# Optimization experiments

Measured on AMD Instinct MI355X. Metric: run time of the kernel, lower is better.

Reference implementation:

```python
import jax, jax.numpy as jnp
import numpy as np

B, H, D, N = 4, 16, 64, 2048

def setup_inputs() -> dict:
    key = jax.random.key(0)
    kq, kk, kv = jax.random.split(key, 3)
    q = jax.random.normal(kq, (B, H, D, N), dtype=jnp.float32)
    k = jax.random.normal(kk, (B, H, D, N), dtype=jnp.float32)
    v = jax.random.normal(kv, (B, H, D, N), dtype=jnp.float32)
    return {"q": q, "k": k, "v": v}

def reference(q, k, v):
    # layout: (b, h, d, n); scale uses head_dim = q.shape[-2]
    scale = q.shape[-2] ** (-0.5)
    sim = jnp.einsum('bhdi,bhdj->bhij', q * scale, k)  # [B,H,N,N]
    attn = jax.nn.softmax(sim, axis=-1)  # stable softmax (internally subtracts max)
    out = jnp.einsum('bhij,bhdj->bhdi', attn, v)  # [B,H,D,N]
    return out
```

## Files before the change

kernel.cpp:

```cpp
#include <hip/hip_runtime.h>


#define DDIM 64
#define NSEQ 2048
#define STR  72
#define BUFB (128 * STR * 2)

typedef _Float16 half8   __attribute__((ext_vector_type(8)));
typedef _Float16 half4v  __attribute__((ext_vector_type(4)));
typedef _Float16 half2v  __attribute__((ext_vector_type(2)));
typedef float    float4v __attribute__((ext_vector_type(4)));

__global__ __launch_bounds__(1024, 4) void attn_fwd(
    const float* __restrict__ qg, const float* __restrict__ kg,
    const float* __restrict__ vg, float* __restrict__ og) {
  __shared__ __align__(16) char smem[4 * BUFB];

  const int t    = threadIdx.x;
  const int lane = t & 63;
  const int w    = t >> 6;
  const int n16  = lane & 15;
  const int quad = lane >> 4;

  const int bid  = blockIdx.x;
  const int head = ((bid & 7) << 3) | (bid >> 5);
  const int tile = (bid >> 3) & 3;
  const int i0   = tile * 512;

  const float* qh = qg + (size_t)head * DDIM * NSEQ;
  const float* kh = kg + (size_t)head * DDIM * NSEQ;
  const float* vh = vg + (size_t)head * DDIM * NSEQ;

  const int  u   = t & 511;
  const bool isK = (t < 512);
  const int  dp  = u & 31;
  const int  iq  = u >> 5;
  const int  vd  = u >> 3;
  const int  sj  = u & 7;
  const int  vg_ = sj >> 2;
  const int  vq  = sj & 3;

  const float* kp  = kh + (2 * dp) * NSEQ + iq * 4;
  const float* vpA = vh + vd * NSEQ + vg_ * 32 + vq * 4;

  float4v ra, rb;
  if (isK) { ra = *(const float4v*)(kp);  rb = *(const float4v*)(kp + NSEQ); }
  else     { ra = *(const float4v*)(vpA); rb = *(const float4v*)(vpA + 16);  }

  {
    _Float16* Qt = (_Float16*)smem;
    const float mul = 0.125f * 1.44269504088896340736f;
    const int dpq = t & 31;
    const int ic  = t >> 5;
#pragma unroll
    for (int h = 0; h < 4; ++h) {
      const float* r0 = qh + (2 * dpq) * NSEQ + i0 + h * 128 + ic * 4;
      float4v a = *(const float4v*)(r0);
      float4v b = *(const float4v*)(r0 + NSEQ);
      _Float16* base = Qt + (h * 128 + ic * 4) * STR + 2 * dpq;
#pragma unroll
      for (int s = 0; s < 4; ++s) {
        half2v hh = {(_Float16)(a[s] * mul), (_Float16)(b[s] * mul)};
        *(half2v*)(base + s * STR) = hh;
      }
    }
  }
  __syncthreads();

  const _Float16* Qt = (const _Float16*)smem;
  half8 bq[2][2];
#pragma unroll
  for (int ig = 0; ig < 2; ++ig) {
    bq[ig][0] = *(const half8*)(Qt + (w * 32 + ig * 16 + n16) * STR + quad * 8);
    bq[ig][1] = *(const half8*)(Qt + (w * 32 + ig * 16 + n16) * STR + 32 + quad * 8);
  }
  __syncthreads();

  const half8 ones = {1.0f16, 1.0f16, 1.0f16, 1.0f16,
                      1.0f16, 1.0f16, 1.0f16, 1.0f16};

  float4v o[2][4];
  float4v lac[2];
#pragma unroll
  for (int ig = 0; ig < 2; ++ig) {
#pragma unroll
    for (int dt = 0; dt < 4; ++dt) o[ig][dt] = (float4v){0.f, 0.f, 0.f, 0.f};
    lac[ig] = (float4v){0.f, 0.f, 0.f, 0.f};
  }

  {
    _Float16* Ktw = (_Float16*)(smem + BUFB);
    if (isK) {
      _Float16* base = Ktw + (iq * 4) * STR + 2 * dp;
#pragma unroll
      for (int s = 0; s < 4; ++s) {
        half2v hh = {(_Float16)ra[s], (_Float16)rb[s]};
        *(half2v*)(base + s * STR) = hh;
      }
    } else {
      half8 hv = {(_Float16)ra[0], (_Float16)ra[1], (_Float16)ra[2], (_Float16)ra[3],
                  (_Float16)rb[0], (_Float16)rb[1], (_Float16)rb[2], (_Float16)rb[3]};
      *(half8*)(Ktw + 64 * STR + vd * STR + sj * 8) = hv;
    }
  }
  __syncthreads();

  for (int kt = 0; kt < 32; ++kt) {
    const _Float16* Kt = (const _Float16*)(smem + ((kt + 1) & 1) * BUFB);
    const _Float16* Vt = Kt + 64 * STR;

    if (kt < 31) {
      const int j1 = (kt + 1) * 64;
      if (isK) { ra = *(const float4v*)(kp + j1); rb = *(const float4v*)(kp + NSEQ + j1); }
      else     { ra = *(const float4v*)(vpA + j1); rb = *(const float4v*)(vpA + j1 + 16); }
    }

    half4v p[2][4];
#pragma unroll
    for (int jt = 0; jt < 4; ++jt) {
      half8 kfa = *(const half8*)(Kt + (jt * 16 + n16) * STR + quad * 8);
      half8 kfb = *(const half8*)(Kt + (jt * 16 + n16) * STR + 32 + quad * 8);
#pragma unroll
      for (int ig = 0; ig < 2; ++ig) {
        float4v sa = {0.f, 0.f, 0.f, 0.f};
        sa = __builtin_amdgcn_mfma_f32_16x16x32_f16(kfa, bq[ig][0], sa, 0, 0, 0);
        sa = __builtin_amdgcn_mfma_f32_16x16x32_f16(kfb, bq[ig][1], sa, 0, 0, 0);
        p[ig][jt] = (half4v){(_Float16)__builtin_amdgcn_exp2f(sa[0]),
                             (_Float16)__builtin_amdgcn_exp2f(sa[1]),
                             (_Float16)__builtin_amdgcn_exp2f(sa[2]),
                             (_Float16)__builtin_amdgcn_exp2f(sa[3])};
      }
    }

    half8 pg[2][2];
#pragma unroll
    for (int ig = 0; ig < 2; ++ig) {
      pg[ig][0] = __builtin_shufflevector(p[ig][0], p[ig][1], 0, 1, 2, 3, 4, 5, 6, 7);
      pg[ig][1] = __builtin_shufflevector(p[ig][2], p[ig][3], 0, 1, 2, 3, 4, 5, 6, 7);
    }

    __builtin_amdgcn_s_setprio(1);
#pragma unroll
    for (int ig = 0; ig < 2; ++ig) {
      lac[ig] = __builtin_amdgcn_mfma_f32_16x16x32_f16(ones, pg[ig][0], lac[ig], 0, 0, 0);
      lac[ig] = __builtin_amdgcn_mfma_f32_16x16x32_f16(ones, pg[ig][1], lac[ig], 0, 0, 0);
    }
#pragma unroll
    for (int dt = 0; dt < 4; ++dt) {
#pragma unroll
      for (int g = 0; g < 2; ++g) {
        half8 vaf = *(const half8*)(Vt + (dt * 16 + n16) * STR + (g * 4 + quad) * 8);
#pragma unroll
        for (int ig = 0; ig < 2; ++ig) {
          o[ig][dt] = __builtin_amdgcn_mfma_f32_16x16x32_f16(
              vaf, pg[ig][g], o[ig][dt], 0, 0, 0);
        }
      }
    }
    __builtin_amdgcn_s_setprio(0);

    if (kt < 31) {
      _Float16* Ktw = (_Float16*)(smem + (kt & 1) * BUFB);
      if (isK) {
        _Float16* base = Ktw + (iq * 4) * STR + 2 * dp;
#pragma unroll
        for (int s = 0; s < 4; ++s) {
          half2v hh = {(_Float16)ra[s], (_Float16)rb[s]};
          *(half2v*)(base + s * STR) = hh;
        }
      } else {
        half8 hv = {(_Float16)ra[0], (_Float16)ra[1], (_Float16)ra[2], (_Float16)ra[3],
                    (_Float16)rb[0], (_Float16)rb[1], (_Float16)rb[2], (_Float16)rb[3]};
        *(half8*)(Ktw + 64 * STR + vd * STR + sj * 8) = hv;
      }
      __syncthreads();
    }
  }

#pragma unroll
  for (int ig = 0; ig < 2; ++ig) {
    const float inv = 1.0f / lac[ig][0];
    float* ob = og + (size_t)head * DDIM * NSEQ + i0 + w * 32 + ig * 16 + n16;
#pragma unroll
    for (int dt = 0; dt < 4; ++dt) {
#pragma unroll
      for (int r = 0; r < 4; ++r) {
        ob[(size_t)(dt * 16 + quad * 4 + r) * NSEQ] = o[ig][dt][r] * inv;
      }
    }
  }
}

extern "C" void kernel_launch(void* const* d_in, const int* in_sizes, int n_in,
                              void* d_out, int out_size, void* d_ws, size_t ws_size,
                              hipStream_t stream) {
  (void)in_sizes; (void)n_in; (void)d_ws; (void)ws_size; (void)out_size;
  const float* q = (const float*)d_in[0];
  const float* k = (const float*)d_in[1];
  const float* v = (const float*)d_in[2];
  attn_fwd<<<dim3(256), dim3(1024), 0, stream>>>(q, k, v, (float*)d_out);
}
```

Baseline: 177.3 us.

## Process two KV tiles per barrier with four-buffer shared-memory pipeline

Restructures the KV loop to load and compute two 64-column K/V tiles per stage, rotating through four shared-memory buffers. This halves the number of block-wide barriers and lets two global loads stay in flight behind two tiles of MFMA work. The cost is double the staging registers (ra..rd) at 1024 threads per block, which raises register pressure and could cause spills.

```diff
diff --git a/kernel.cpp b/kernel.cpp
--- a/kernel.cpp
+++ b/kernel.cpp
@@ -10,6 +10,78 @@
 typedef _Float16 half4v  __attribute__((ext_vector_type(4)));
 typedef _Float16 half2v  __attribute__((ext_vector_type(2)));
 typedef float    float4v __attribute__((ext_vector_type(4)));
+
+#define LOADT(J1, RA, RB)                                                   \
+  do {                                                                      \
+    if (isK) { RA = *(const float4v*)(kp + (J1));                           \
+               RB = *(const float4v*)(kp + NSEQ + (J1)); }                  \
+    else     { RA = *(const float4v*)(vpA + (J1));                          \
+               RB = *(const float4v*)(vpA + (J1) + 16); }                   \
+  } while (0)
+
+#define WTILE(BUF, RA, RB)                                                  \
+  do {                                                                      \
+    _Float16* Ktw_ = (_Float16*)(BUF);                                      \
+    if (isK) {                                                              \
+      _Float16* base_ = Ktw_ + (iq * 4) * STR + 2 * dp;                     \
+      _Pragma("unroll")                                                     \
+      for (int s_ = 0; s_ < 4; ++s_) {                                      \
+        half2v hh_ = {(_Float16)RA[s_], (_Float16)RB[s_]};                  \
+        *(half2v*)(base_ + s_ * STR) = hh_;                                 \
+      }                                                                     \
+    } else {                                                                \
+      half8 hv_ = {(_Float16)RA[0], (_Float16)RA[1], (_Float16)RA[2],       \
+                   (_Float16)RA[3], (_Float16)RB[0], (_Float16)RB[1],       \
+                   (_Float16)RB[2], (_Float16)RB[3]};                       \
+      *(half8*)(Ktw_ + 64 * STR + vd * STR + sj * 8) = hv_;                 \
+    }                                                                       \
+  } while (0)
+
+#define CTILE(KBUF)                                                         \
+  do {                                                                      \
+    const _Float16* Kt_ = (const _Float16*)(KBUF);                          \
+    const _Float16* Vt_ = Kt_ + 64 * STR;                                   \
+    half4v p_[2][4];                                                        \
+    _Pragma("unroll")                                                       \
+    for (int jt = 0; jt < 4; ++jt) {                                        \
+      half8 kfa = *(const half8*)(Kt_ + (jt * 16 + n16) * STR + quad * 8);  \
+      half8 kfb = *(const half8*)(Kt_ + (jt * 16 + n16) * STR + 32 + quad * 8); \
+      _Pragma("unroll")                                                     \
+      for (int ig = 0; ig < 2; ++ig) {                                      \
+        float4v sa = {0.f, 0.f, 0.f, 0.f};                                  \
+        sa = __builtin_amdgcn_mfma_f32_16x16x32_f16(kfa, bq[ig][0], sa, 0, 0, 0); \
+        sa = __builtin_amdgcn_mfma_f32_16x16x32_f16(kfb, bq[ig][1], sa, 0, 0, 0); \
+        p_[ig][jt] = (half4v){(_Float16)__builtin_amdgcn_exp2f(sa[0]),      \
+                              (_Float16)__builtin_amdgcn_exp2f(sa[1]),      \
+                              (_Float16)__builtin_amdgcn_exp2f(sa[2]),      \
+                              (_Float16)__builtin_amdgcn_exp2f(sa[3])};     \
+      }                                                                     \
+    }                                                                       \
+    half8 pg_[2][2];                                                        \
+    _Pragma("unroll")                                                       \
+    for (int ig = 0; ig < 2; ++ig) {                                        \
+      pg_[ig][0] = __builtin_shufflevector(p_[ig][0], p_[ig][1], 0, 1, 2, 3, 4, 5, 6, 7); \
+      pg_[ig][1] = __builtin_shufflevector(p_[ig][2], p_[ig][3], 0, 1, 2, 3, 4, 5, 6, 7); \
+    }                                                                       \
+    __builtin_amdgcn_s_setprio(1);                                          \
+    _Pragma("unroll")                                                       \
+    for (int ig = 0; ig < 2; ++ig) {                                        \
+      lac[ig] = __builtin_amdgcn_mfma_f32_16x16x32_f16(ones, pg_[ig][0], lac[ig], 0, 0, 0); \
+      lac[ig] = __builtin_amdgcn_mfma_f32_16x16x32_f16(ones, pg_[ig][1], lac[ig], 0, 0, 0); \
+    }                                                                       \
+    _Pragma("unroll")                                                       \
+    for (int dt = 0; dt < 4; ++dt) {                                        \
+      _Pragma("unroll")                                                     \
+      for (int g = 0; g < 2; ++g) {                                         \
+        half8 vaf = *(const half8*)(Vt_ + (dt * 16 + n16) * STR + (g * 4 + quad) * 8); \
+        _Pragma("unroll")                                                   \
+        for (int ig = 0; ig < 2; ++ig) {                                    \
+          o[ig][dt] = __builtin_amdgcn_mfma_f32_16x16x32_f16(vaf, pg_[ig][g], o[ig][dt], 0, 0, 0); \
+        }                                                                   \
+      }                                                                     \
+    }                                                                       \
+    __builtin_amdgcn_s_setprio(0);                                          \
+  } while (0)
 
 __global__ __launch_bounds__(1024, 4) void attn_fwd(
     const float* __restrict__ qg, const float* __restrict__ kg,
@@ -43,9 +115,14 @@
   const float* kp  = kh + (2 * dp) * NSEQ + iq * 4;
   const float* vpA = vh + vd * NSEQ + vg_ * 32 + vq * 4;
 
-  float4v ra, rb;
-  if (isK) { ra = *(const float4v*)(kp);  rb = *(const float4v*)(kp + NSEQ); }
-  else     { ra = *(const float4v*)(vpA); rb = *(const float4v*)(vpA + 16);  }
+  char* const Bb0 = smem;
+  char* const Bb1 = smem + BUFB;
+  char* const Bb2 = smem + 2 * BUFB;
+  char* const Bb3 = smem + 3 * BUFB;
+
+  float4v ra, rb, rc, rd;
+  LOADT(0, ra, rb);
+  LOADT(64, rc, rd);
 
   {
     _Float16* Qt = (_Float16*)smem;
@@ -76,6 +153,10 @@
   }
   __syncthreads();
 
+  WTILE(Bb1, ra, rb);
+  WTILE(Bb2, rc, rd);
+  __syncthreads();
+
   const half8 ones = {1.0f16, 1.0f16, 1.0f16, 1.0f16,
                       1.0f16, 1.0f16, 1.0f16, 1.0f16};
 
@@ -88,91 +169,26 @@
     lac[ig] = (float4v){0.f, 0.f, 0.f, 0.f};
   }
 
-  {
-    _Float16* Ktw = (_Float16*)(smem + BUFB);
-    if (isK) {
-      _Float16* base = Ktw + (iq * 4) * STR + 2 * dp;
-#pragma unroll
-      for (int s = 0; s < 4; ++s) {
-        half2v hh = {(_Float16)ra[s], (_Float16)rb[s]};
-        *(half2v*)(base + s * STR) = hh;
-      }
-    } else {
-      half8 hv = {(_Float16)ra[0], (_Float16)ra[1], (_Float16)ra[2], (_Float16)ra[3],
-                  (_Float16)rb[0], (_Float16)rb[1], (_Float16)rb[2], (_Float16)rb[3]};
-      *(half8*)(Ktw + 64 * STR + vd * STR + sj * 8) = hv;
-    }
-  }
-  __syncthreads();
-
-  for (int kt = 0; kt < 32; ++kt) {
-    const _Float16* Kt = (const _Float16*)(smem + ((kt + 1) & 1) * BUFB);
-    const _Float16* Vt = Kt + 64 * STR;
-
-    if (kt < 31) {
-      const int j1 = (kt + 1) * 64;
-      if (isK) { ra = *(const float4v*)(kp + j1); rb = *(const float4v*)(kp + NSEQ + j1); }
-      else     { ra = *(const float4v*)(vpA + j1); rb = *(const float4v*)(vpA + j1 + 16); }
-    }
-
-    half4v p[2][4];
-#pragma unroll
-    for (int jt = 0; jt < 4; ++jt) {
-      half8 kfa = *(const half8*)(Kt + (jt * 16 + n16) * STR + quad * 8);
-      half8 kfb = *(const half8*)(Kt + (jt * 16 + n16) * STR + 32 + quad * 8);
-#pragma unroll
-      for (int ig = 0; ig < 2; ++ig) {
-        float4v sa = {0.f, 0.f, 0.f, 0.f};
-        sa = __builtin_amdgcn_mfma_f32_16x16x32_f16(kfa, bq[ig][0], sa, 0, 0, 0);
-        sa = __builtin_amdgcn_mfma_f32_16x16x32_f16(kfb, bq[ig][1], sa, 0, 0, 0);
-        p[ig][jt] = (half4v){(_Float16)__builtin_amdgcn_exp2f(sa[0]),
-                             (_Float16)__builtin_amdgcn_exp2f(sa[1]),
-                             (_Float16)__builtin_amdgcn_exp2f(sa[2]),
-                             (_Float16)__builtin_amdgcn_exp2f(sa[3])};
-      }
-    }
-
-    half8 pg[2][2];
-#pragma unroll
-    for (int ig = 0; ig < 2; ++ig) {
-      pg[ig][0] = __builtin_shufflevector(p[ig][0], p[ig][1], 0, 1, 2, 3, 4, 5, 6, 7);
-      pg[ig][1] = __builtin_shufflevector(p[ig][2], p[ig][3], 0, 1, 2, 3, 4, 5, 6, 7);
-    }
-
-    __builtin_amdgcn_s_setprio(1);
-#pragma unroll
-    for (int ig = 0; ig < 2; ++ig) {
-      lac[ig] = __builtin_amdgcn_mfma_f32_16x16x32_f16(ones, pg[ig][0], lac[ig], 0, 0, 0);
-      lac[ig] = __builtin_amdgcn_mfma_f32_16x16x32_f16(ones, pg[ig][1], lac[ig], 0, 0, 0);
-    }
-#pragma unroll
-    for (int dt = 0; dt < 4; ++dt) {
-#pragma unroll
-      for (int g = 0; g < 2; ++g) {
-        half8 vaf = *(const half8*)(Vt + (dt * 16 + n16) * STR + (g * 4 + quad) * 8);
-#pragma unroll
-        for (int ig = 0; ig < 2; ++ig) {
-          o[ig][dt] = __builtin_amdgcn_mfma_f32_16x16x32_f16(
-              vaf, pg[ig][g], o[ig][dt], 0, 0, 0);
-        }
-      }
-    }
-    __builtin_amdgcn_s_setprio(0);
-
-    if (kt < 31) {
-      _Float16* Ktw = (_Float16*)(smem + (kt & 1) * BUFB);
-      if (isK) {
-        _Float16* base = Ktw + (iq * 4) * STR + 2 * dp;
-#pragma unroll
-        for (int s = 0; s < 4; ++s) {
-          half2v hh = {(_Float16)ra[s], (_Float16)rb[s]};
-          *(half2v*)(base + s * STR) = hh;
-        }
-      } else {
-        half8 hv = {(_Float16)ra[0], (_Float16)ra[1], (_Float16)ra[2], (_Float16)ra[3],
-                    (_Float16)rb[0], (_Float16)rb[1], (_Float16)rb[2], (_Float16)rb[3]};
-        *(half8*)(Ktw + 64 * STR + vd * STR + sj * 8) = hv;
-      }
+#pragma unroll 1
+  for (int m = 0; m < 8; ++m) {
+    const int bt = m * 4;
+    LOADT((bt + 2) * 64, ra, rb);
+    LOADT((bt + 3) * 64, rc, rd);
+    CTILE(Bb1);
+    CTILE(Bb2);
+    WTILE(Bb3, ra, rb);
+    WTILE(Bb0, rc, rd);
+    __syncthreads();
+
+    if (m < 7) {
+      LOADT((bt + 4) * 64, ra, rb);
+      LOADT((bt + 5) * 64, rc, rd);
+    }
+    CTILE(Bb3);
+    CTILE(Bb0);
+    if (m < 7) {
+      WTILE(Bb1, ra, rb);
+      WTILE(Bb2, rc, rd);
       __syncthreads();
     }
   }
```

After: 205.7 us. 16.1% more time.
